# Optimization experiments

Measured on AMD Instinct MI355X. Metric: run time of the kernel, lower is better.

Reference implementation:

```python
import jax, jax.numpy as jnp
import numpy as np

N = 50000      # nodes
E = 800000     # edges (avg degree 16)
D_IN, D_H, D_OUT = 128, 128, 64


def setup_inputs() -> dict:
    key = jax.random.key(0)
    ks = jax.random.split(key, 12)
    s = 0.05  # weight init scale
    return {
        "x": jax.random.normal(ks[0], (N, D_IN), jnp.float32),
        "edge_index": jax.random.randint(ks[1], (2, E), 0, N, dtype=jnp.int64),
        "Wl0": jax.random.normal(ks[2], (D_H, D_IN), jnp.float32) * s,
        "bl0": jax.random.normal(ks[3], (D_H,), jnp.float32) * s,
        "Wr0": jax.random.normal(ks[4], (D_H, D_IN), jnp.float32) * s,
        "Wl1": jax.random.normal(ks[5], (D_H, D_H), jnp.float32) * s,
        "bl1": jax.random.normal(ks[6], (D_H,), jnp.float32) * s,
        "Wr1": jax.random.normal(ks[7], (D_H, D_H), jnp.float32) * s,
        "Wl2": jax.random.normal(ks[8], (D_OUT, D_H), jnp.float32) * s,
        "bl2": jax.random.normal(ks[9], (D_OUT,), jnp.float32) * s,
        "Wr2": jax.random.normal(ks[10], (D_OUT, D_H), jnp.float32) * s,
    }


def _sage_layer(h, src, dst, Wl, bl, Wr):
    # mean aggregation over incoming neighbors: out[i] = mean_{j in N(i)} h[j]
    n = h.shape[0]
    agg = jax.ops.segment_sum(h[src], dst, num_segments=n)          # [N, D]
    deg = jax.ops.segment_sum(jnp.ones((src.shape[0],), h.dtype), dst,
                              num_segments=n)                        # [N]
    mean = agg / jnp.maximum(deg, 1.0)[:, None]  # empty rows -> 0, matches torch_sparse
    # lin_l(agg) + lin_r(self); lin_r has no bias in PyG SAGEConv
    return mean @ Wl.T + bl + h @ Wr.T


def reference(x, edge_index, Wl0, bl0, Wr0, Wl1, bl1, Wr1, Wl2, bl2, Wr2):
    src, dst = edge_index[1], edge_index[0]  # adj row = dst, col = src
    h = jax.nn.relu(_sage_layer(x, src, dst, Wl0, bl0, Wr0))
    h = jax.nn.relu(_sage_layer(h, src, dst, Wl1, bl1, Wr1))
    h = _sage_layer(h, src, dst, Wl2, bl2, Wr2)
    return jax.nn.log_softmax(h, axis=1)
```

## Files before the change

kernel.cpp:

```cpp
#include <hip/hip_runtime.h>
#include <hip/hip_bf16.h>


typedef __attribute__((ext_vector_type(8))) short bf16x8;
typedef __attribute__((ext_vector_type(4))) float f32x4;

#define NPB 128
#define BCAP 2560
#define EPB 8192
#define EPT 32
#define CPAD 16

__device__ __forceinline__ unsigned short f2bf(float f) {
    unsigned int u = __builtin_bit_cast(unsigned int, f);
    u += 0x7fffu + ((u >> 16) & 1u);
    return (unsigned short)(u >> 16);
}
__device__ __forceinline__ float bf2f(unsigned int bits16) {
    return __builtin_bit_cast(float, bits16 << 16);
}


__global__ __launch_bounds__(256) void dist_cast_kernel(
        const int* __restrict__ dst, const int* __restrict__ srcv,
        int* __restrict__ gcnt, unsigned int* __restrict__ staging, int E, int NBc,
        const float* __restrict__ x,
        const float* p0, const float* p1, const float* p2,
        const float* p3, const float* p4, const float* p5,
        unsigned short* __restrict__ xbf, unsigned short* __restrict__ wbf,
        int xpairs, int distBlocks) {
    __shared__ unsigned int stage[EPB];
    __shared__ int hist[400];
    __shared__ int lstart[400];
    __shared__ int gbase[400];
    __shared__ int scanbuf[256];
    int t = threadIdx.x;

    if (blockIdx.x >= distBlocks) {
        int bid = blockIdx.x - distBlocks;
        int xblocks = (xpairs + 255) / 256;
        if (bid < xblocks) {
            int i = bid * 256 + t;
            if (i < xpairs) {
                float2 v = ((const float2*)x)[i];
                unsigned int p = (unsigned int)f2bf(v.x) | ((unsigned int)f2bf(v.y) << 16);
                ((unsigned int*)xbf)[i] = p;
            }
        } else {
            int w = (bid - xblocks) * 256 + t;
            if (w < 40960) {
                const float* src;
                int local;
                if      (w < 8192)  { src = p0; local = w; }
                else if (w < 16384) { src = p1; local = w - 8192; }
                else if (w < 24576) { src = p2; local = w - 16384; }
                else if (w < 32768) { src = p3; local = w - 24576; }
                else if (w < 36864) { src = p4; local = w - 32768; }
                else                { src = p5; local = w - 36864; }
                float2 v = ((const float2*)src)[local];
                unsigned int p = (unsigned int)f2bf(v.x) | ((unsigned int)f2bf(v.y) << 16);
                ((unsigned int*)wbf)[w] = p;
            }
        }
        return;
    }

    int e0 = blockIdx.x * EPB;
    unsigned int w[EPT];

    for (int b = t; b < NBc + 1; b += 256) hist[b] = 0;
    __syncthreads();

#pragma unroll
    for (int i = 0; i < EPT; ++i) {
        int e = e0 + i * 256 + t;
        unsigned int word = 0xFFFFFFFFu;
        if (e < E) word = ((unsigned int)dst[e] << 16) | (unsigned int)srcv[e];
        w[i] = word;
        int b = (int)(word >> 23); if (b > NBc) b = NBc;
        atomicAdd(&hist[b], 1);
    }
    __syncthreads();

    int b0 = 2 * t, b1 = 2 * t + 1;
    int h0 = (b0 <= NBc) ? hist[b0] : 0;
    int h1 = (b1 <= NBc) ? hist[b1] : 0;
    int pair = h0 + h1;
    scanbuf[t] = pair;
    __syncthreads();
    for (int off = 1; off < 256; off <<= 1) {
        int v = (t >= off) ? scanbuf[t - off] : 0;
        __syncthreads();
        scanbuf[t] += v;
        __syncthreads();
    }
    int excl = scanbuf[t] - pair;
    if (b0 <= NBc) lstart[b0] = excl;
    if (b1 <= NBc) lstart[b1] = excl + h0;
    __syncthreads();

    for (int b = t; b < NBc; b += 256) {
        int h = hist[b];
        gbase[b] = h ? atomicAdd(&gcnt[b * CPAD], h) : 0;
    }
    for (int b = t; b < NBc + 1; b += 256) hist[b] = lstart[b];
    __syncthreads();

#pragma unroll
    for (int i = 0; i < EPT; ++i) {
        unsigned int word = w[i];
        int b = (int)(word >> 23); if (b > NBc) b = NBc;
        int p = atomicAdd(&hist[b], 1);
        stage[p] = word;
    }
    __syncthreads();

    int total = lstart[NBc];
    for (int i = t; i < total; i += 256) {
        unsigned int word = stage[i];
        int b = (int)(word >> 23);
        int gpos = gbase[b] + (i - lstart[b]);
        staging[(size_t)b * BCAP + gpos] = word;
    }
}


__device__ __forceinline__ void gemm_tile(const unsigned short* __restrict__ H,
                                          const unsigned short* __restrict__ Wl,
                                          const unsigned short* __restrict__ Wr,
                                          unsigned short* __restrict__ CL,
                                          unsigned short* __restrict__ CR,
                                          int bx, int y, int half, int ldC, int N) {
    int wave = threadIdx.x >> 6;
    int lane = threadIdx.x & 63;
    int l15 = lane & 15, quad = lane >> 4;
    const unsigned short* W = (y < half) ? Wl : Wr;
    unsigned short* Cout = (y < half) ? CL : CR;
    int slab = (y < half) ? y : y - half;
    int wrow0 = slab * 64;
    int col0 = slab * 64;
    int m0 = bx * 128 + wave * 32;

    int r0 = m0 + l15;      if (r0 > N - 1) r0 = N - 1;
    int r1 = m0 + 16 + l15; if (r1 > N - 1) r1 = N - 1;
    const bf16x8* A0 = (const bf16x8*)(H + (size_t)r0 * 128);
    const bf16x8* A1 = (const bf16x8*)(H + (size_t)r1 * 128);

    f32x4 acc[2][4] = {};
#pragma unroll
    for (int ks = 0; ks < 4; ++ks) {
        int vidx = ks * 4 + quad;
        bf16x8 a0 = A0[vidx];
        bf16x8 a1 = A1[vidx];
#pragma unroll
        for (int j = 0; j < 4; ++j) {
            const bf16x8* B = (const bf16x8*)(W + (size_t)(wrow0 + j * 16 + l15) * 128);
            bf16x8 b = B[vidx];
            acc[0][j] = __builtin_amdgcn_mfma_f32_16x16x32_bf16(a0, b, acc[0][j], 0, 0, 0);
            acc[1][j] = __builtin_amdgcn_mfma_f32_16x16x32_bf16(a1, b, acc[1][j], 0, 0, 0);
        }
    }

#pragma unroll
    for (int i = 0; i < 2; ++i)
#pragma unroll
        for (int j = 0; j < 4; ++j)
#pragma unroll
            for (int r = 0; r < 4; ++r) {
                int row = m0 + i * 16 + quad * 4 + r;
                if (row < N) {
                    int col = col0 + j * 16 + l15;
                    Cout[(size_t)row * ldC + col] = f2bf(acc[i][j][r]);
                }
            }
}

__global__ __launch_bounds__(256) void gemm_kernel(const unsigned short* __restrict__ H,
                                                   const unsigned short* __restrict__ Wl,
                                                   const unsigned short* __restrict__ Wr,
                                                   unsigned short* __restrict__ CL,
                                                   unsigned short* __restrict__ CR,
                                                   int half, int ldC, int N) {
    gemm_tile(H, Wl, Wr, CL, CR, blockIdx.x, blockIdx.y, half, ldC, N);
}


__global__ __launch_bounds__(256) void build_gemm0_kernel(
        const unsigned int* __restrict__ staging, const int* __restrict__ gcnt,
        int* __restrict__ row_ptr, int* __restrict__ adj, int N, int NBc,
        const unsigned short* __restrict__ xbf,
        const unsigned short* __restrict__ wl0, const unsigned short* __restrict__ wr0,
        unsigned short* __restrict__ CL, unsigned short* __restrict__ CR,
        int gemmRows) {
    __shared__ int lstart[400];
    __shared__ int scanbuf[256];
    __shared__ int hist[NPB];
    __shared__ int scn[NPB];
    int t = threadIdx.x;

    if (blockIdx.x >= (unsigned)NBc) {
        int g = blockIdx.x - NBc;
        gemm_tile(xbf, wl0, wr0, CL, CR, g % gemmRows, g / gemmRows, 2, 128, N);
        return;
    }
    int b = blockIdx.x;

    int b0 = 2 * t, b1 = 2 * t + 1;
    int h0 = (b0 < NBc) ? gcnt[b0 * CPAD] : 0;
    int h1 = (b1 < NBc) ? gcnt[b1 * CPAD] : 0;
    int pair = h0 + h1;
    scanbuf[t] = pair;
    __syncthreads();
    for (int off = 1; off < 256; off <<= 1) {
        int v = (t >= off) ? scanbuf[t - off] : 0;
        __syncthreads();
        scanbuf[t] += v;
        __syncthreads();
    }
    int excl = scanbuf[t] - pair;
    if (b0 < NBc) lstart[b0] = excl;
    if (b1 < NBc) lstart[b1] = excl + h0;
    if (b == 0 && t == 255) row_ptr[N] = scanbuf[255];
    __syncthreads();

    int n0 = b * NPB;
    int nb = N - n0; if (nb > NPB) nb = NPB;
    int ec = gcnt[b * CPAD];
    int bb = lstart[b];
    const unsigned int* st = staging + (size_t)b * BCAP;

    if (t < NPB) hist[t] = 0;
    __syncthreads();
    for (int i = t; i < ec; i += 256)
        atomicAdd(&hist[(st[i] >> 16) & (NPB - 1)], 1);
    __syncthreads();

    int v = (t < NPB) ? hist[t] : 0;
    if (t < NPB) scn[t] = v;
    __syncthreads();
    for (int off = 1; off < NPB; off <<= 1) {
        int u = (t >= off && t < NPB) ? scn[t - off] : 0;
        __syncthreads();
        if (t < NPB) scn[t] += u;
        __syncthreads();
    }
    if (t < NPB) hist[t] = scn[t] - v;
    if (t < nb) row_ptr[n0 + t] = bb + (scn[t] - v);
    __syncthreads();

    for (int i = t; i < ec; i += 256) {
        unsigned int pk = st[i];
        int p = atomicAdd(&hist[(pk >> 16) & (NPB - 1)], 1);
        adj[bb + p] = (int)(pk & 0xffffu);
    }
}


__global__ __launch_bounds__(256) void agg_relu_kernel(const unsigned short* __restrict__ CL,
                                                       const unsigned short* __restrict__ CR,
                                                       const int* __restrict__ row_ptr,
                                                       const int* __restrict__ adj,
                                                       const float* __restrict__ bias,
                                                       unsigned short* __restrict__ hout, int N) {
    int node = (int)((blockIdx.x * blockDim.x + threadIdx.x) >> 6);
    int lane = threadIdx.x & 63;
    if (node >= N) return;
    int beg = row_ptr[node], end = row_ptr[node + 1];
    float sx[4] = {}, sy[4] = {};

    int e = beg;
    while (e < end) {
        int cnt = end - e; if (cnt > 64) cnt = 64;
        int c1 = cnt - 1;
        int ll = lane > c1 ? c1 : lane;
        int myidx = adj[e + ll];

        for (int i = 0; i < cnt; i += 16) {
            int rem = cnt - i;
            unsigned int v[16];
#pragma unroll
            for (int j = 0; j < 16; ++j) {
                int tt = i + j; if (tt > c1) tt = c1;
                int s = __shfl(myidx, tt);
                v[j] = ((const unsigned int*)(CL + (size_t)s * 128))[lane];
            }
#pragma unroll
            for (int j = 0; j < 16; ++j) {
                float m = (j < rem) ? 1.f : 0.f;
                sx[j & 3] += m * bf2f(v[j] & 0xffffu);
                sy[j & 3] += m * bf2f(v[j] >> 16);
            }
        }
        e += cnt;
    }

    float fx = (sx[0] + sx[1]) + (sx[2] + sx[3]);
    float fy = (sy[0] + sy[1]) + (sy[2] + sy[3]);
    int deg = end - beg;
    float inv = 1.0f / (float)(deg > 1 ? deg : 1);
    float2 bb = ((const float2*)bias)[lane];
    unsigned int rv = ((const unsigned int*)(CR + (size_t)node * 128))[lane];
    float ox = fmaxf(fx * inv + bb.x + bf2f(rv & 0xffffu), 0.f);
    float oy = fmaxf(fy * inv + bb.y + bf2f(rv >> 16), 0.f);
    unsigned int p = (unsigned int)f2bf(ox) | ((unsigned int)f2bf(oy) << 16);
    ((unsigned int*)(hout + (size_t)node * 128))[lane] = p;
}


__global__ __launch_bounds__(256) void final_kernel(const unsigned short* __restrict__ CL,
                                                    const unsigned short* __restrict__ CR,
                                                    const int* __restrict__ row_ptr,
                                                    const int* __restrict__ adj,
                                                    const float* __restrict__ bias,
                                                    float* __restrict__ out, int N) {
    int node = (int)((blockIdx.x * blockDim.x + threadIdx.x) >> 6);
    int lane = threadIdx.x & 63;
    if (node >= N) return;
    int beg = row_ptr[node], end = row_ptr[node + 1];
    float a[4] = {};

    int e = beg;
    while (e < end) {
        int cnt = end - e; if (cnt > 64) cnt = 64;
        int c1 = cnt - 1;
        int ll = lane > c1 ? c1 : lane;
        int myidx = adj[e + ll];

        for (int i = 0; i < cnt; i += 16) {
            int rem = cnt - i;
            float v[16];
#pragma unroll
            for (int j = 0; j < 16; ++j) {
                int tt = i + j; if (tt > c1) tt = c1;
                int s = __shfl(myidx, tt);
                v[j] = bf2f((unsigned int)CL[(size_t)s * 64 + lane]);
            }
#pragma unroll
            for (int j = 0; j < 16; ++j) {
                float m = (j < rem) ? 1.f : 0.f;
                a[j & 3] += m * v[j];
            }
        }
        e += cnt;
    }

    float sum = (a[0] + a[1]) + (a[2] + a[3]);
    int deg = end - beg;
    float inv = 1.0f / (float)(deg > 1 ? deg : 1);
    float u = sum * inv + bias[lane] + bf2f((unsigned int)CR[(size_t)node * 64 + lane]);

    float m = u;
#pragma unroll
    for (int off = 32; off > 0; off >>= 1) m = fmaxf(m, __shfl_xor(m, off));
    float ex = __expf(u - m);
    float se = ex;
#pragma unroll
    for (int off = 32; off > 0; off >>= 1) se += __shfl_xor(se, off);
    out[(size_t)node * 64 + lane] = (u - m) - __logf(se);
}


extern "C" void kernel_launch(void* const* d_in, const int* in_sizes, int n_in,
                              void* d_out, int out_size, void* d_ws, size_t ws_size,
                              hipStream_t stream) {
    const float* x   = (const float*)d_in[0];
    const int*   ei  = (const int*)d_in[1];
    const float* Wl0 = (const float*)d_in[2];
    const float* bl0 = (const float*)d_in[3];
    const float* Wr0 = (const float*)d_in[4];
    const float* Wl1 = (const float*)d_in[5];
    const float* bl1 = (const float*)d_in[6];
    const float* Wr1 = (const float*)d_in[7];
    const float* Wl2 = (const float*)d_in[8];
    const float* bl2 = (const float*)d_in[9];
    const float* Wr2 = (const float*)d_in[10];
    float* out = (float*)d_out;

    const int N  = in_sizes[0] / 128;
    const int E  = in_sizes[1] / 2;
    const int NB = (N + NPB - 1) / NPB;

    char* ws = (char*)d_ws;
    auto alloc = [&](size_t bytes) {
        char* p = ws;
        ws += (bytes + 255) & ~(size_t)255;
        return p;
    };
    int*   row_ptr = (int*)alloc((size_t)(N + 1) * 4);
    int*   adj     = (int*)alloc((size_t)E * 4);
    int*   gcnt    = (int*)alloc((size_t)NB * CPAD * 4);
    unsigned int* staging = (unsigned int*)alloc((size_t)NB * BCAP * 4);
    unsigned short* xbf = (unsigned short*)alloc((size_t)N * 128 * 2);
    unsigned short* wbf = (unsigned short*)alloc((size_t)81920 * 2);
    unsigned short* CLb = (unsigned short*)alloc((size_t)N * 128 * 2);
    unsigned short* CRb = (unsigned short*)alloc((size_t)N * 128 * 2);
    unsigned short* hA  = (unsigned short*)alloc((size_t)N * 128 * 2);
    unsigned short* hB  = (unsigned short*)alloc((size_t)N * 128 * 2);

    const int* dstp = ei;
    const int* srcp = ei + E;

    hipMemsetAsync(gcnt, 0, (size_t)NB * CPAD * 4, stream);

    int distBlocks = (E + EPB - 1) / EPB;
    int xpairs = N * 64;
    int castBlocks = (xpairs + 255) / 256 + 160;
    dist_cast_kernel<<<distBlocks + castBlocks, 256, 0, stream>>>(
        dstp, srcp, gcnt, staging, E, NB,
        x, Wl0, Wr0, Wl1, Wr1, Wl2, Wr2, xbf, wbf, xpairs, distBlocks);

    unsigned short* wl0 = wbf;
    unsigned short* wr0 = wbf + 16384;
    unsigned short* wl1 = wbf + 32768;
    unsigned short* wr1 = wbf + 49152;
    unsigned short* wl2 = wbf + 65536;
    unsigned short* wr2 = wbf + 73728;

    dim3 blk(256);
    int gemmRows = (N + 127) / 128;
    int aggBlocks = (N * 64 + 255) / 256;

    build_gemm0_kernel<<<NB + gemmRows * 4, blk, 0, stream>>>(
        staging, gcnt, row_ptr, adj, N, NB, xbf, wl0, wr0, CLb, CRb, gemmRows);

    agg_relu_kernel<<<aggBlocks, blk, 0, stream>>>(CLb, CRb, row_ptr, adj, bl0, hA, N);
    gemm_kernel<<<dim3(gemmRows, 4), blk, 0, stream>>>(hA, wl1, wr1, CLb, CRb, 2, 128, N);
    agg_relu_kernel<<<aggBlocks, blk, 0, stream>>>(CLb, CRb, row_ptr, adj, bl1, hB, N);
    gemm_kernel<<<dim3(gemmRows, 2), blk, 0, stream>>>(hB, wl2, wr2, CLb, CRb, 1, 64, N);
    final_kernel<<<aggBlocks, blk, 0, stream>>>(CLb, CRb, row_ptr, adj, bl2, out, N);
}
```

Measured before the change: 278.2 us.

## Fuse neighbor aggregation+ReLU with next-layer GEMM via LDS tile

Replaces the separate agg_relu and gemm kernels with one kernel. Each 128-node block aggregates neighbors two nodes at a time per wave, with the next node pair's adjacency prefetched, and writes the bf16 activations into a padded LDS tile. After a barrier it runs the MFMA GEMM for the next layer straight from LDS. This removes the global round trip of the hidden activations and two kernel launches. The cost is a much smaller grid (one block per 128 nodes instead of one wave per node), so there is less parallelism for the latency-bound gather, plus separate ping-pong output buffers.

New measurement: 323.7 us. 16.3% more time.

```diff
diff --git a/kernel.cpp b/kernel.cpp
--- a/kernel.cpp
+++ b/kernel.cpp
@@ -10,6 +10,7 @@
 #define EPB 8192
 #define EPT 32
 #define CPAD 16
+#define HS_STRIDE_U32 68
 
 __device__ __forceinline__ unsigned short f2bf(float f) {
     unsigned int u = __builtin_bit_cast(unsigned int, f);
@@ -175,15 +176,6 @@
             }
 }
 
-__global__ __launch_bounds__(256) void gemm_kernel(const unsigned short* __restrict__ H,
-                                                   const unsigned short* __restrict__ Wl,
-                                                   const unsigned short* __restrict__ Wr,
-                                                   unsigned short* __restrict__ CL,
-                                                   unsigned short* __restrict__ CR,
-                                                   int half, int ldC, int N) {
-    gemm_tile(H, Wl, Wr, CL, CR, blockIdx.x, blockIdx.y, half, ldC, N);
-}
-
 
 __global__ __launch_bounds__(256) void build_gemm0_kernel(
         const unsigned int* __restrict__ staging, const int* __restrict__ gcnt,
@@ -256,54 +248,188 @@
 }
 
 
-__global__ __launch_bounds__(256) void agg_relu_kernel(const unsigned short* __restrict__ CL,
-                                                       const unsigned short* __restrict__ CR,
-                                                       const int* __restrict__ row_ptr,
-                                                       const int* __restrict__ adj,
-                                                       const float* __restrict__ bias,
-                                                       unsigned short* __restrict__ hout, int N) {
-    int node = (int)((blockIdx.x * blockDim.x + threadIdx.x) >> 6);
+__global__ __launch_bounds__(256) void agg_gemm_kernel(
+        const unsigned short* __restrict__ CLin, const unsigned short* __restrict__ CRin,
+        const int* __restrict__ row_ptr, const int* __restrict__ adj,
+        const float* __restrict__ bias,
+        const unsigned short* __restrict__ Wl, const unsigned short* __restrict__ Wr,
+        unsigned short* __restrict__ CLout, unsigned short* __restrict__ CRout,
+        int N, int E, int ldOut, int slabsPerSide) {
+    __shared__ unsigned int HsU[128 * HS_STRIDE_U32];
+
+    int wave = threadIdx.x >> 6;
     int lane = threadIdx.x & 63;
-    if (node >= N) return;
-    int beg = row_ptr[node], end = row_ptr[node + 1];
-    float sx[4] = {}, sy[4] = {};
-
-    int e = beg;
-    while (e < end) {
-        int cnt = end - e; if (cnt > 64) cnt = 64;
-        int c1 = cnt - 1;
-        int ll = lane > c1 ? c1 : lane;
-        int myidx = adj[e + ll];
-
-        for (int i = 0; i < cnt; i += 16) {
-            int rem = cnt - i;
-            unsigned int v[16];
-#pragma unroll
-            for (int j = 0; j < 16; ++j) {
-                int tt = i + j; if (tt > c1) tt = c1;
-                int s = __shfl(myidx, tt);
-                v[j] = ((const unsigned int*)(CL + (size_t)s * 128))[lane];
-            }
-#pragma unroll
-            for (int j = 0; j < 16; ++j) {
-                float m = (j < rem) ? 1.f : 0.f;
-                sx[j & 3] += m * bf2f(v[j] & 0xffffu);
-                sy[j & 3] += m * bf2f(v[j] >> 16);
-            }
-        }
-        e += cnt;
-    }
-
-    float fx = (sx[0] + sx[1]) + (sx[2] + sx[3]);
-    float fy = (sy[0] + sy[1]) + (sy[2] + sy[3]);
-    int deg = end - beg;
-    float inv = 1.0f / (float)(deg > 1 ? deg : 1);
-    float2 bb = ((const float2*)bias)[lane];
-    unsigned int rv = ((const unsigned int*)(CR + (size_t)node * 128))[lane];
-    float ox = fmaxf(fx * inv + bb.x + bf2f(rv & 0xffffu), 0.f);
-    float oy = fmaxf(fy * inv + bb.y + bf2f(rv >> 16), 0.f);
-    unsigned int p = (unsigned int)f2bf(ox) | ((unsigned int)f2bf(oy) << 16);
-    ((unsigned int*)(hout + (size_t)node * 128))[lane] = p;
+    int base = blockIdx.x * 128 + wave * 32;
+
+    int rpidx = base + lane; if (rpidx > N) rpidx = N;
+    int rp = row_ptr[rpidx];
+
+    auto ldadj = [&](int b, int e_) {
+        int cnt = e_ - b;
+        int ll = lane; if (ll > cnt - 1) ll = cnt - 1; if (ll < 0) ll = 0;
+        int ai = b + ll; if (ai > E - 1) ai = E - 1; if (ai < 0) ai = 0;
+        return adj[ai];
+    };
+
+    int begA = __shfl(rp, 0), endA = __shfl(rp, 1);
+    int begB = __shfl(rp, 1), endB = __shfl(rp, 2);
+    int adjA = ldadj(begA, endA);
+    int adjB = ldadj(begB, endB);
+
+    for (int k = 0; k < 32; k += 2) {
+        int bA = begA, eA = endA, curA = adjA;
+        int bB = begB, eB = endB, curB = adjB;
+        if (k + 2 < 32) {
+            begA = __shfl(rp, k + 2); endA = __shfl(rp, k + 3);
+            begB = __shfl(rp, k + 3); endB = __shfl(rp, k + 4);
+            adjA = ldadj(begA, endA);
+            adjB = ldadj(begB, endB);
+        }
+
+        float sxA[4] = {}, syA[4] = {}, sxB[4] = {}, syB[4] = {};
+        int cA = eA - bA; if (cA > 64) cA = 64;
+        int cB = eB - bB; if (cB > 64) cB = 64;
+        int c1A = cA - 1, c1B = cB - 1;
+        int cmax = cA > cB ? cA : cB;
+
+        for (int i = 0; i < cmax; i += 16) {
+            unsigned int vA[16], vB[16];
+            if (i < cA) {
+#pragma unroll
+                for (int j = 0; j < 16; ++j) {
+                    int tt = i + j; if (tt > c1A) tt = c1A;
+                    int s = __shfl(curA, tt);
+                    vA[j] = ((const unsigned int*)(CLin + (size_t)s * 128))[lane];
+                }
+            }
+            if (i < cB) {
+#pragma unroll
+                for (int j = 0; j < 16; ++j) {
+                    int tt = i + j; if (tt > c1B) tt = c1B;
+                    int s = __shfl(curB, tt);
+                    vB[j] = ((const unsigned int*)(CLin + (size_t)s * 128))[lane];
+                }
+            }
+            if (i < cA) {
+                int rem = cA - i;
+#pragma unroll
+                for (int j = 0; j < 16; ++j) {
+                    float m = (j < rem) ? 1.f : 0.f;
+                    sxA[j & 3] += m * bf2f(vA[j] & 0xffffu);
+                    syA[j & 3] += m * bf2f(vA[j] >> 16);
+                }
+            }
+            if (i < cB) {
+                int rem = cB - i;
+#pragma unroll
+                for (int j = 0; j < 16; ++j) {
+                    float m = (j < rem) ? 1.f : 0.f;
+                    sxB[j & 3] += m * bf2f(vB[j] & 0xffffu);
+                    syB[j & 3] += m * bf2f(vB[j] >> 16);
+                }
+            }
+        }
+
+        for (int half2 = 0; half2 < 2; ++half2) {
+            int bb_ = half2 ? bB : bA, ee_ = half2 ? eB : eA;
+            float* sx = half2 ? sxB : sxA;
+            float* sy = half2 ? syB : syA;
+            int e = bb_ + 64;
+            while (e < ee_) {
+                int cnt = ee_ - e; if (cnt > 64) cnt = 64;
+                int c1 = cnt - 1;
+                int ll = lane > c1 ? c1 : lane;
+                int myidx = adj[e + ll];
+                for (int i = 0; i < cnt; i += 16) {
+                    int rem = cnt - i;
+                    unsigned int v[16];
+#pragma unroll
+                    for (int j = 0; j < 16; ++j) {
+                        int tt = i + j; if (tt > c1) tt = c1;
+                        int s = __shfl(myidx, tt);
+                        v[j] = ((const unsigned int*)(CLin + (size_t)s * 128))[lane];
+                    }
+#pragma unroll
+                    for (int j = 0; j < 16; ++j) {
+                        float m = (j < rem) ? 1.f : 0.f;
+                        sx[j & 3] += m * bf2f(v[j] & 0xffffu);
+                        sy[j & 3] += m * bf2f(v[j] >> 16);
+                    }
+                }
+                e += cnt;
+            }
+        }
+
+        float2 bb2 = ((const float2*)bias)[lane];
+#pragma unroll
+        for (int half2 = 0; half2 < 2; ++half2) {
+            int node = base + k + half2;
+            float fx, fy; int deg;
+            if (half2 == 0) {
+                fx = (sxA[0] + sxA[1]) + (sxA[2] + sxA[3]);
+                fy = (syA[0] + syA[1]) + (syA[2] + syA[3]);
+                deg = eA - bA;
+            } else {
+                fx = (sxB[0] + sxB[1]) + (sxB[2] + sxB[3]);
+                fy = (syB[0] + syB[1]) + (syB[2] + syB[3]);
+                deg = eB - bB;
+            }
+            unsigned int pk = 0;
+            if (node < N) {
+                float inv = 1.0f / (float)(deg > 1 ? deg : 1);
+                unsigned int rv = ((const unsigned int*)(CRin + (size_t)node * 128))[lane];
+                float ox = fmaxf(fx * inv + bb2.x + bf2f(rv & 0xffffu), 0.f);
+                float oy = fmaxf(fy * inv + bb2.y + bf2f(rv >> 16), 0.f);
+                pk = (unsigned int)f2bf(ox) | ((unsigned int)f2bf(oy) << 16);
+            }
+            HsU[(size_t)(wave * 32 + k + half2) * HS_STRIDE_U32 + lane] = pk;
+        }
+    }
+
+    __syncthreads();
+
+    int l15 = lane & 15, quad = lane >> 4;
+    int slabId, rowOff, passes;
+    if (slabsPerSide == 2) { slabId = wave; rowOff = 0; passes = 4; }
+    else                   { slabId = wave >> 1; rowOff = (wave & 1) * 64; passes = 2; }
+    const unsigned short* W;
+    unsigned short* Cout;
+    int slab;
+    if (slabId < slabsPerSide) { W = Wl; Cout = CLout; slab = slabId; }
+    else                       { W = Wr; Cout = CRout; slab = slabId - slabsPerSide; }
+    int wrow0 = slab * 64, col0 = slab * 64;
+    int m0 = blockIdx.x * 128;
+    const unsigned short* HsB = (const unsigned short*)HsU;
+
+    for (int p = 0; p < passes; ++p) {
+        int ml = rowOff + p * 32;
+        f32x4 acc[2][4] = {};
+#pragma unroll
+        for (int ks = 0; ks < 4; ++ks) {
+            int vidx = ks * 4 + quad;
+            bf16x8 a0 = *(const bf16x8*)(HsB + (size_t)(ml + l15) * (HS_STRIDE_U32 * 2) + vidx * 8);
+            bf16x8 a1 = *(const bf16x8*)(HsB + (size_t)(ml + 16 + l15) * (HS_STRIDE_U32 * 2) + vidx * 8);
+#pragma unroll
+            for (int j = 0; j < 4; ++j) {
+                const bf16x8* B = (const bf16x8*)(W + (size_t)(wrow0 + j * 16 + l15) * 128);
+                bf16x8 b = B[vidx];
+                acc[0][j] = __builtin_amdgcn_mfma_f32_16x16x32_bf16(a0, b, acc[0][j], 0, 0, 0);
+                acc[1][j] = __builtin_amdgcn_mfma_f32_16x16x32_bf16(a1, b, acc[1][j], 0, 0, 0);
+            }
+        }
+#pragma unroll
+        for (int i = 0; i < 2; ++i)
+#pragma unroll
+            for (int j = 0; j < 4; ++j)
+#pragma unroll
+                for (int r = 0; r < 4; ++r) {
+                    int row = m0 + ml + i * 16 + quad * 4 + r;
+                    if (row < N) {
+                        int col = col0 + j * 16 + l15;
+                        Cout[(size_t)row * ldOut + col] = f2bf(acc[i][j][r]);
+                    }
+                }
+    }
 }
 
 
@@ -392,10 +518,12 @@
     unsigned int* staging = (unsigned int*)alloc((size_t)NB * BCAP * 4);
     unsigned short* xbf = (unsigned short*)alloc((size_t)N * 128 * 2);
     unsigned short* wbf = (unsigned short*)alloc((size_t)81920 * 2);
-    unsigned short* CLb = (unsigned short*)alloc((size_t)N * 128 * 2);
-    unsigned short* CRb = (unsigned short*)alloc((size_t)N * 128 * 2);
-    unsigned short* hA  = (unsigned short*)alloc((size_t)N * 128 * 2);
-    unsigned short* hB  = (unsigned short*)alloc((size_t)N * 128 * 2);
+    unsigned short* CL0 = (unsigned short*)alloc((size_t)N * 128 * 2);
+    unsigned short* CR0 = (unsigned short*)alloc((size_t)N * 128 * 2);
+    unsigned short* CL1 = (unsigned short*)alloc((size_t)N * 128 * 2);
+    unsigned short* CR1 = (unsigned short*)alloc((size_t)N * 128 * 2);
+    unsigned short* CL2 = (unsigned short*)alloc((size_t)N * 64 * 2);
+    unsigned short* CR2 = (unsigned short*)alloc((size_t)N * 64 * 2);
 
     const int* dstp = ei;
     const int* srcp = ei + E;
@@ -421,11 +549,13 @@
     int aggBlocks = (N * 64 + 255) / 256;
 
     build_gemm0_kernel<<<NB + gemmRows * 4, blk, 0, stream>>>(
-        staging, gcnt, row_ptr, adj, N, NB, xbf, wl0, wr0, CLb, CRb, gemmRows);
-
-    agg_relu_kernel<<<aggBlocks, blk, 0, stream>>>(CLb, CRb, row_ptr, adj, bl0, hA, N);
-    gemm_kernel<<<dim3(gemmRows, 4), blk, 0, stream>>>(hA, wl1, wr1, CLb, CRb, 2, 128, N);
-    agg_relu_kernel<<<aggBlocks, blk, 0, stream>>>(CLb, CRb, row_ptr, adj, bl1, hB, N);
-    gemm_kernel<<<dim3(gemmRows, 2), blk, 0, stream>>>(hB, wl2, wr2, CLb, CRb, 1, 64, N);
-    final_kernel<<<aggBlocks, blk, 0, stream>>>(CLb, CRb, row_ptr, adj, bl2, out, N);
-}
+        staging, gcnt, row_ptr, adj, N, NB, xbf, wl0, wr0, CL0, CR0, gemmRows);
+
+    agg_gemm_kernel<<<gemmRows, blk, 0, stream>>>(
+        CL0, CR0, row_ptr, adj, bl0, wl1, wr1, CL1, CR1, N, E, 128, 2);
+
+    agg_gemm_kernel<<<gemmRows, blk, 0, stream>>>(
+        CL1, CR1, row_ptr, adj, bl1, wl2, wr2, CL2, CR2, N, E, 64, 1);
+
+    final_kernel<<<aggBlocks, blk, 0, stream>>>(CL2, CR2, row_ptr, adj, bl2, out, N);
+}
```
